# Optimization experiments

Hardware: AMD Instinct MI355X
Metric: run time of the kernel (lower is better)

Reference implementation:

```python
import jax, jax.numpy as jnp
import numpy as np
import math

B, L, D, H, FF = 8, 4096, 1024, 16, 4
BELOW, ABOVE = 1, 1
DH = D // H


def _timing_signal(length, channels, min_ts=1.0, max_ts=10000.0):
    position = np.arange(length)
    num_timescales = channels // 2
    log_inc = math.log(max_ts / min_ts) / (num_timescales - 1)
    inv = min_ts * np.exp(np.arange(num_timescales).astype(float) * -log_inc)
    scaled = position[:, None] * inv[None, :]
    sig = np.zeros((length, channels))
    sig[:, 0::2] = np.sin(scaled)
    sig[:, 1::2] = np.cos(scaled)
    return jnp.asarray(sig[None], dtype=jnp.float32)  # [1, L, D]


def setup_inputs() -> dict:
    key = jax.random.key(0)
    ks = jax.random.split(key, 8)
    s = lambda k, sh: jax.random.normal(k, sh, jnp.float32) * 0.02
    return dict(
        X=jax.random.normal(ks[0], (B, L, D), jnp.float32),
        src_mask=jnp.zeros((B, L), jnp.bool_),  # True = padding
        pe=_timing_signal(L, D),
        Wq=s(ks[1], (D, D)), Wk=s(ks[2], (D, D)), Wv=s(ks[3], (D, D)),
        bq=jnp.zeros((D,), jnp.float32), bk=jnp.zeros((D,), jnp.float32), bv=jnp.zeros((D,), jnp.float32),
        Wo=s(ks[4], (D, D)), bo=jnp.zeros((D,), jnp.float32),
        g1=jnp.ones((D,), jnp.float32), beta1=jnp.zeros((D,), jnp.float32),
        W1=s(ks[5], (D, FF * D)), b1=jnp.zeros((FF * D,), jnp.float32),
        W2=s(ks[6], (FF * D, D)), b2=jnp.zeros((D,), jnp.float32),
        g2=jnp.ones((D,), jnp.float32), beta2=jnp.zeros((D,), jnp.float32),
    )


def _layernorm(x, g, b, eps=1e-5):
    m = x.mean(-1, keepdims=True)
    v = ((x - m) ** 2).mean(-1, keepdims=True)
    return (x - m) * jax.lax.rsqrt(v + eps) * g + b


def reference(X, src_mask, pe, Wq, Wk, Wv, bq, bk, bv, Wo, bo,
              g1, beta1, W1, b1, W2, b2, g2, beta2):
    # positional encoding (dropout is identity in eval)
    X = X + pe  # [B, L, D]

    # QKV projections -> [B, L, H, DH]
    q = (X @ Wq + bq).reshape(B, L, H, DH)
    k = (X @ Wk + bk).reshape(B, L, H, DH)
    v = (X @ Wv + bv).reshape(B, L, H, DH)

    # Banded (diagonal-window) attention: query i attends keys i-BELOW..i+ABOVE.
    Wwin = BELOW + ABOVE + 1
    idx = jnp.arange(L)[:, None] + jnp.arange(-BELOW, ABOVE + 1)[None, :]  # [L, Wwin]
    valid = (idx >= 0) & (idx < L)
    idxc = jnp.clip(idx, 0, L - 1)
    kw = k[:, idxc]  # [B, L, Wwin, H, DH]
    vw = v[:, idxc]

    scores = jnp.einsum('blhd,blwhd->bhlw', q, kw) / jnp.sqrt(jnp.float32(DH))
    key_ok = ~src_mask  # [B, L]
    allow = valid[None, :, :] & key_ok[:, idxc]  # [B, L, Wwin]
    scores = jnp.where(allow[:, None, :, :], scores, jnp.float32(-1e30))
    attn = jax.nn.softmax(scores, axis=-1)  # [B, H, L, Wwin]
    ctx = jnp.einsum('bhlw,blwhd->blhd', attn, vw).reshape(B, L, D)
    Xt = ctx @ Wo + bo

    # post-norm residual blocks (dropout identity in eval)
    X = _layernorm(X + Xt, g1, beta1)
    ffn = jnp.maximum(X @ W1 + b1, 0.0) @ W2 + b2
    X = _layernorm(X + ffn, g2, beta2)
    return X
```

## Files before the change

### kernel.cpp

```cpp
#include <hip/hip_runtime.h>
#include <hip/hip_bf16.h>

#define B_  8
#define L_  4096
#define D_  1024
#define H_  16
#define MTOT (B_*L_)
#define NFF  (4*D_)

typedef __bf16 bf16_t;
typedef float  f32x4 __attribute__((ext_vector_type(4)));
typedef __bf16 b16x8 __attribute__((ext_vector_type(8)));
typedef __bf16 b16x4 __attribute__((ext_vector_type(4)));

#define OFF_WQKVT ((size_t)0)
#define OFF_WOT   ((size_t)6291456)
#define OFF_W1T   ((size_t)8388608)
#define OFF_W2T   ((size_t)16777216)
#define OFF_BQKV  ((size_t)25165824)
#define OFF_XB    ((size_t)33554432)
#define OFF_B     ((size_t)100663296)

__global__ __launch_bounds__(256) void k_add_pe(const float* __restrict__ X,
                                                const float* __restrict__ pe,
                                                bf16_t* __restrict__ Xb)
{
    size_t i  = ((size_t)blockIdx.x * 256 + threadIdx.x) * 4;
    size_t ld = i & ((size_t)L_ * D_ - 1);
    float4 x = *(const float4*)(X + i);
    float4 p = *(const float4*)(pe + ld);
    b16x4 b;
    b[0] = (bf16_t)(x.x + p.x); b[1] = (bf16_t)(x.y + p.y);
    b[2] = (bf16_t)(x.z + p.z); b[3] = (bf16_t)(x.w + p.w);
    *(b16x4*)(Xb + i) = b;
}

__global__ __launch_bounds__(256) void k_prep(const float* __restrict__ Wq,
                                              const float* __restrict__ Wk,
                                              const float* __restrict__ Wv,
                                              const float* __restrict__ Wo,
                                              const float* __restrict__ W1,
                                              const float* __restrict__ W2,
                                              const float* __restrict__ bq,
                                              const float* __restrict__ bk,
                                              const float* __restrict__ bv,
                                              bf16_t* __restrict__ WqkvT,
                                              bf16_t* __restrict__ WoT,
                                              bf16_t* __restrict__ W1T,
                                              bf16_t* __restrict__ W2T,
                                              float* __restrict__ bqkv)
{
    const int id = blockIdx.x;
    if (id >= 12288) {
        const int i = (id - 12288) * 256 + threadIdx.x;
        if (i < 1024)       bqkv[i] = bq[i];
        else if (i < 2048)  bqkv[i] = bk[i - 1024];
        else if (i < 3072)  bqkv[i] = bv[i - 2048];
        return;
    }
    const float* src; bf16_t* dst; int K, N, t;
    if (id < 4096) {
        const int w = id >> 10; t = id & 1023; K = 1024; N = 1024;
        src = (w == 0) ? Wq : (w == 1) ? Wk : (w == 2) ? Wv : Wo;
        dst = (w < 3) ? (WqkvT + (size_t)w * 1024 * 1024) : WoT;
    } else if (id < 8192) {
        t = id - 4096; K = 1024; N = 4096; src = W1; dst = W1T;
    } else {
        t = id - 8192; K = 4096; N = 1024; src = W2; dst = W2T;
    }
    const int ntiles = N >> 5;
    const int n0 = (t % ntiles) << 5;
    const int k0 = (t / ntiles) << 5;

    __shared__ float tt[32][33];
    const int tx = threadIdx.x & 31;
    const int ty = threadIdx.x >> 5;
    #pragma unroll
    for (int i = ty; i < 32; i += 8)
        tt[i][tx] = src[(size_t)(k0 + i) * N + n0 + tx];
    __syncthreads();
    #pragma unroll
    for (int i = ty; i < 32; i += 8)
        dst[(size_t)(n0 + i) * K + k0 + tx] = (bf16_t)tt[tx][i];
}

#define BM 128
#define BN 128
#define BK 64

__device__ __forceinline__ void gload_lds16(const void* g, char* lds_byte) {
    __builtin_amdgcn_global_load_lds((const __attribute__((address_space(1))) void*)g,
                                     (__attribute__((address_space(3))) void*)lds_byte,
                                     16, 0, 0);
}

template<int EPI>
__global__ __launch_bounds__(256, 4) void k_gemm_bt(const bf16_t* __restrict__ A,
                                                    const bf16_t* __restrict__ Bt,
                                                    const float* __restrict__ bias,
                                                    void* __restrict__ Cv,
                                                    const int N, const int K)
{
    __shared__ __align__(16) bf16_t As[BM * BK];
    __shared__ __align__(16) bf16_t Bs[BN * BK];
    const int tid  = threadIdx.x;
    const int wave = tid >> 6;
    const int lane = tid & 63;

    const int Nt = gridDim.x, Mt = gridDim.y;
    const int lid = blockIdx.y * Nt + blockIdx.x;
    int bm, bn;
    {
        const int xcd = lid & 7;
        const int s   = lid >> 3;
        bm = xcd * (Mt >> 3) + s / Nt;
        bn = s % Nt;
    }
    const int n0 = bn * BN;
    const int m0 = bm * BM;
    const int waveM = wave >> 1;
    const int waveN = wave & 1;

    const int srow   = tid >> 3;
    const int schunk = (tid & 7) ^ (srow & 7);
    const bf16_t* ag = A  + (size_t)(m0 + srow) * K + schunk * 8;
    const bf16_t* bg = Bt + (size_t)(n0 + srow) * K + schunk * 8;
    const size_t rstep = (size_t)32 * K;
    char* ldsA = (char*)&As[0] + wave * 1024;
    char* ldsB = (char*)&Bs[0] + wave * 1024;

    const int q   = lane >> 4;
    const int x7  = lane & 7;
    const int sl0 = ((q)     ^ x7) << 3;
    const int sl1 = ((4 + q) ^ x7) << 3;
    const bf16_t* AsP = As + (waveM * 64 + (lane & 15)) * BK;
    const bf16_t* BsP = Bs + (waveN * 64 + (lane & 15)) * BK;

    f32x4 acc[4][4] = {};

    for (int kt = 0; kt < K; kt += BK) {
        __syncthreads();
        #pragma unroll
        for (int c = 0; c < 4; ++c) {
            gload_lds16(ag + c * rstep, ldsA + c * 4096);
            gload_lds16(bg + c * rstep, ldsB + c * 4096);
        }
        ag += BK; bg += BK;
        __syncthreads();
        b16x8 af[4], bfr[4];
        #pragma unroll
        for (int i = 0; i < 4; ++i) af[i]  = *(const b16x8*)(AsP + i * 16 * BK + sl0);
        #pragma unroll
        for (int i = 0; i < 4; ++i) bfr[i] = *(const b16x8*)(BsP + i * 16 * BK + sl0);
        #pragma unroll
        for (int mi = 0; mi < 4; ++mi)
            #pragma unroll
            for (int ni = 0; ni < 4; ++ni)
                acc[mi][ni] = __builtin_amdgcn_mfma_f32_16x16x32_bf16(af[mi], bfr[ni], acc[mi][ni], 0, 0, 0);
        #pragma unroll
        for (int i = 0; i < 4; ++i) af[i]  = *(const b16x8*)(AsP + i * 16 * BK + sl1);
        #pragma unroll
        for (int i = 0; i < 4; ++i) bfr[i] = *(const b16x8*)(BsP + i * 16 * BK + sl1);
        #pragma unroll
        for (int mi = 0; mi < 4; ++mi)
            #pragma unroll
            for (int ni = 0; ni < 4; ++ni)
                acc[mi][ni] = __builtin_amdgcn_mfma_f32_16x16x32_bf16(af[mi], bfr[ni], acc[mi][ni], 0, 0, 0);
    }

    const int rbase = m0 + waveM * 64 + ((lane >> 4) << 2);
    const int cbase = n0 + waveN * 64 + (lane & 15);
    #pragma unroll
    for (int mi = 0; mi < 4; ++mi) {
        #pragma unroll
        for (int ni = 0; ni < 4; ++ni) {
            const int col = cbase + ni * 16;
            const float bb = bias[col];
            #pragma unroll
            for (int r = 0; r < 4; ++r) {
                const int rowg = rbase + mi * 16 + r;
                float v = acc[mi][ni][r] + bb;
                if (EPI == 2) v = fmaxf(v, 0.0f);
                if (EPI == 0) ((float*)Cv)[(size_t)rowg * N + col] = v;
                else          ((bf16_t*)Cv)[(size_t)rowg * N + col] = (bf16_t)v;
            }
        }
    }
}

__global__ __launch_bounds__(256) void k_attn(const bf16_t* __restrict__ QKV,
                                              const unsigned char* __restrict__ mask,
                                              bf16_t* __restrict__ ctx)
{
    const int wid  = (blockIdx.x << 2) + (threadIdx.x >> 6);
    const int lane = threadIdx.x & 63;
    const int h    = wid & (H_ - 1);
    const int l    = wid >> 4;
    const int lb   = l & (L_ - 1);

    const float qv = (float)QKV[(size_t)l * 3072 + h * 64 + lane];
    float sc[3], vv[3];
    bool  ok[3];
    #pragma unroll
    for (int w = 0; w < 3; ++w) {
        const int d   = w - 1;
        const bool valid = (unsigned)(lb + d) < (unsigned)L_;
        const int dc  = valid ? d : 0;
        const size_t rb = (size_t)(l + dc) * 3072 + h * 64 + lane;
        const float kk = (float)QKV[rb + 1024];
        vv[w] = (float)QKV[rb + 2048];
        ok[w] = valid && (mask[l + dc] == 0);
        sc[w] = qv * kk;
    }
    #pragma unroll
    for (int off = 32; off; off >>= 1) {
        sc[0] += __shfl_xor(sc[0], off);
        sc[1] += __shfl_xor(sc[1], off);
        sc[2] += __shfl_xor(sc[2], off);
    }
    const float s0 = ok[0] ? sc[0] * 0.125f : -1e30f;
    const float s1 = ok[1] ? sc[1] * 0.125f : -1e30f;
    const float s2 = ok[2] ? sc[2] * 0.125f : -1e30f;
    const float mx = fmaxf(s0, fmaxf(s1, s2));
    const float e0 = __expf(s0 - mx), e1 = __expf(s1 - mx), e2 = __expf(s2 - mx);
    const float inv = 1.0f / (e0 + e1 + e2);
    const float o = (e0 * vv[0] + e1 * vv[1] + e2 * vv[2]) * inv;
    ctx[(size_t)l * 1024 + h * 64 + lane] = (bf16_t)o;
}

template<int FINAL>
__global__ __launch_bounds__(256) void k_res_ln(const bf16_t* __restrict__ Xres,
                                                const float* __restrict__ Y,
                                                const float* __restrict__ g,
                                                const float* __restrict__ beta,
                                                bf16_t* __restrict__ outB,
                                                float* __restrict__ outF)
{
    const int row = blockIdx.x;
    const int tid = threadIdx.x;
    const size_t base = (size_t)row * D_ + tid * 4;
    b16x4  xr = *(const b16x4*)(Xres + base);
    float4 y  = *(const float4*)(Y + base);
    const float t0 = (float)xr[0] + y.x, t1 = (float)xr[1] + y.y;
    const float t2 = (float)xr[2] + y.z, t3 = (float)xr[3] + y.w;
    float s = t0 + t1 + t2 + t3;
    float q = t0*t0 + t1*t1 + t2*t2 + t3*t3;
    #pragma unroll
    for (int off = 32; off; off >>= 1) {
        s += __shfl_xor(s, off);
        q += __shfl_xor(q, off);
    }
    __shared__ float red[8];
    const int wv = tid >> 6, ln = tid & 63;
    if (ln == 0) { red[wv] = s; red[wv + 4] = q; }
    __syncthreads();
    s = red[0] + red[1] + red[2] + red[3];
    q = red[4] + red[5] + red[6] + red[7];
    const float mean = s * (1.0f / D_);
    const float var  = q * (1.0f / D_) - mean * mean;
    const float rs   = rsqrtf(var + 1e-5f);
    const int c = tid * 4;
    float4 gv = *(const float4*)(g + c);
    float4 bv = *(const float4*)(beta + c);
    float o0 = (t0 - mean) * rs * gv.x + bv.x;
    float o1 = (t1 - mean) * rs * gv.y + bv.y;
    float o2 = (t2 - mean) * rs * gv.z + bv.z;
    float o3 = (t3 - mean) * rs * gv.w + bv.w;
    if (FINAL) {
        float4 o; o.x = o0; o.y = o1; o.z = o2; o.w = o3;
        *(float4*)(outF + base) = o;
    } else {
        b16x4 b; b[0] = (bf16_t)o0; b[1] = (bf16_t)o1; b[2] = (bf16_t)o2; b[3] = (bf16_t)o3;
        *(b16x4*)(outB + base) = b;
    }
}

extern "C" void kernel_launch(void* const* d_in, const int* in_sizes, int n_in,
                              void* d_out, int out_size, void* d_ws, size_t ws_size,
                              hipStream_t stream)
{
    const float* X    = (const float*)d_in[0];
    const unsigned char* mask = (const unsigned char*)d_in[1];
    const float* pe   = (const float*)d_in[2];
    const float* Wq   = (const float*)d_in[3];
    const float* Wk   = (const float*)d_in[4];
    const float* Wv   = (const float*)d_in[5];
    const float* bq   = (const float*)d_in[6];
    const float* bk   = (const float*)d_in[7];
    const float* bv   = (const float*)d_in[8];
    const float* Wo   = (const float*)d_in[9];
    const float* bo   = (const float*)d_in[10];
    const float* g1   = (const float*)d_in[11];
    const float* be1  = (const float*)d_in[12];
    const float* W1   = (const float*)d_in[13];
    const float* b1   = (const float*)d_in[14];
    const float* W2   = (const float*)d_in[15];
    const float* b2   = (const float*)d_in[16];
    const float* g2   = (const float*)d_in[17];
    const float* be2  = (const float*)d_in[18];

    char* ws = (char*)d_ws;
    bf16_t* WqkvT = (bf16_t*)(ws + OFF_WQKVT);
    bf16_t* WoT   = (bf16_t*)(ws + OFF_WOT);
    bf16_t* W1T   = (bf16_t*)(ws + OFF_W1T);
    bf16_t* W2T   = (bf16_t*)(ws + OFF_W2T);
    float*  bqkv  = (float*) (ws + OFF_BQKV);
    bf16_t* Xb    = (bf16_t*)(ws + OFF_XB);
    float*  Y     = (float*)d_out;

    const bool big = ws_size >= (size_t)234881024;

    k_add_pe<<<MTOT * D_ / 1024, 256, 0, stream>>>(X, pe, Xb);

    k_prep<<<12300, 256, 0, stream>>>(Wq, Wk, Wv, Wo, W1, W2, bq, bk, bv,
                                      WqkvT, WoT, W1T, W2T, bqkv);

    if (big) {
        bf16_t* ctx  = (bf16_t*)(ws + OFF_B);
        bf16_t* qkvc = (bf16_t*)(ws + OFF_B + 67108864);
        for (int c = 0; c < 4; ++c) {
            const size_t r0 = (size_t)c * 8192;
            k_gemm_bt<1><<<dim3(3072/BN, 8192/BM), 256, 0, stream>>>(
                Xb + r0*D_, WqkvT, bqkv, qkvc, 3072, 1024);
            k_attn<<<8192*H_/4, 256, 0, stream>>>(qkvc, mask + r0, ctx + r0*D_);
        }
        k_gemm_bt<0><<<dim3(1024/BN, MTOT/BM), 256, 0, stream>>>(ctx, WoT, bo, Y, 1024, 1024);
        k_res_ln<0><<<MTOT, 256, 0, stream>>>(Xb, Y, g1, be1, Xb, nullptr);
        bf16_t* hb = (bf16_t*)(ws + OFF_B);
        for (int c = 0; c < 2; ++c) {
            const size_t r0 = (size_t)c * 16384;
            k_gemm_bt<2><<<dim3(NFF/BN, 16384/BM), 256, 0, stream>>>(
                Xb + r0*D_, W1T, b1, hb, NFF, 1024);
            k_gemm_bt<0><<<dim3(1024/BN, 16384/BM), 256, 0, stream>>>(
                hb, W2T, b2, Y + r0*D_, 1024, NFF);
        }
        k_res_ln<1><<<MTOT, 256, 0, stream>>>(Xb, Y, g2, be2, nullptr, (float*)d_out);
    } else {
        bf16_t* qkvc = (bf16_t*)(ws + OFF_B);
        bf16_t* ctxc = (bf16_t*)(ws + OFF_B + 25165824);
        for (int b = 0; b < B_; ++b) {
            const size_t r0 = (size_t)b * L_;
            k_gemm_bt<1><<<dim3(3072/BN, L_/BM), 256, 0, stream>>>(
                Xb + r0*D_, WqkvT, bqkv, qkvc, 3072, 1024);
            k_attn<<<L_*H_/4, 256, 0, stream>>>(qkvc, mask + r0, ctxc);
            k_gemm_bt<0><<<dim3(1024/BN, L_/BM), 256, 0, stream>>>(
                ctxc, WoT, bo, Y + r0*D_, 1024, 1024);
        }
        k_res_ln<0><<<MTOT, 256, 0, stream>>>(Xb, Y, g1, be1, Xb, nullptr);
        bf16_t* hb = (bf16_t*)(ws + OFF_B);
        for (int c = 0; c < 8; ++c) {
            const size_t r0 = (size_t)c * L_;
            k_gemm_bt<2><<<dim3(NFF/BN, L_/BM), 256, 0, stream>>>(
                Xb + r0*D_, W1T, b1, hb, NFF, 1024);
            k_gemm_bt<0><<<dim3(1024/BN, L_/BM), 256, 0, stream>>>(
                hb, W2T, b2, Y + r0*D_, 1024, NFF);
        }
        k_res_ln<1><<<MTOT, 256, 0, stream>>>(Xb, Y, g2, be2, nullptr, (float*)d_out);
    }
}
```

Measured before the change: 1.459 ms.

## Replace GEMM with 256x256 double-buffered ping-pong kernel with priority scheduling

Replaces the 128x128 single-buffered GEMM with a 256x256 tile kernel using 8 waves and 128KB of dynamic LDS. The K loop is double-buffered and split into quarter-phases, so global-to-LDS loads overlap MFMA work, with barriers and s_setprio to order the waves. The goal is more data reuse per tile and hidden load latency, at the cost of lower occupancy and tight manual vmcnt synchronisation. It also adds a one-time attribute setup for the large shared-memory size.

Result: faster. 1.332 ms (-8.7%).

```diff
diff --git a/kernel.cpp b/kernel.cpp
--- a/kernel.cpp
+++ b/kernel.cpp
@@ -84,9 +84,6 @@
         dst[(size_t)(n0 + i) * K + k0 + tx] = (bf16_t)tt[tx][i];
 }
 
-#define BM 128
-#define BN 128
-#define BK 64
 
 __device__ __forceinline__ void gload_lds16(const void* g, char* lds_byte) {
     __builtin_amdgcn_global_load_lds((const __attribute__((address_space(1))) void*)g,
@@ -94,84 +91,105 @@
                                      16, 0, 0);
 }
 
+#define GBAR() __builtin_amdgcn_s_barrier()
+#define VM4()  asm volatile("s_waitcnt vmcnt(4)" ::: "memory")
+#define PRI(x) __builtin_amdgcn_s_setprio(x)
+
 template<int EPI>
-__global__ __launch_bounds__(256, 4) void k_gemm_bt(const bf16_t* __restrict__ A,
-                                                    const bf16_t* __restrict__ Bt,
-                                                    const float* __restrict__ bias,
-                                                    void* __restrict__ Cv,
-                                                    const int N, const int K)
-{
-    __shared__ __align__(16) bf16_t As[BM * BK];
-    __shared__ __align__(16) bf16_t Bs[BN * BK];
+__global__ __launch_bounds__(512, 2) void k_g256(const bf16_t* __restrict__ A,
+                                                 const bf16_t* __restrict__ Bt,
+                                                 const float* __restrict__ bias,
+                                                 void* __restrict__ Cv,
+                                                 const int N, const int K)
+{
+    extern __shared__ char smem[];
     const int tid  = threadIdx.x;
     const int wave = tid >> 6;
     const int lane = tid & 63;
+    const int wm   = wave >> 2;
+    const int wn   = wave & 3;
 
     const int Nt = gridDim.x, Mt = gridDim.y;
     const int lid = blockIdx.y * Nt + blockIdx.x;
-    int bm, bn;
-    {
-        const int xcd = lid & 7;
-        const int s   = lid >> 3;
-        bm = xcd * (Mt >> 3) + s / Nt;
-        bn = s % Nt;
-    }
-    const int n0 = bn * BN;
-    const int m0 = bm * BM;
-    const int waveM = wave >> 1;
-    const int waveN = wave & 1;
+    const int xcd = lid & 7;
+    const int sgl = lid >> 3;
+    const int bm  = xcd * (Mt >> 3) + sgl / Nt;
+    const int bn  = sgl % Nt;
+    const int m0 = bm * 256, n0 = bn * 256;
 
     const int srow   = tid >> 3;
     const int schunk = (tid & 7) ^ (srow & 7);
-    const bf16_t* ag = A  + (size_t)(m0 + srow) * K + schunk * 8;
-    const bf16_t* bg = Bt + (size_t)(n0 + srow) * K + schunk * 8;
-    const size_t rstep = (size_t)32 * K;
-    char* ldsA = (char*)&As[0] + wave * 1024;
-    char* ldsB = (char*)&Bs[0] + wave * 1024;
-
-    const int q   = lane >> 4;
-    const int x7  = lane & 7;
-    const int sl0 = ((q)     ^ x7) << 3;
+    const bf16_t* agA = A  + (size_t)(m0 + srow) * K + schunk * 8;
+    const bf16_t* bgB = Bt + (size_t)(n0 + srow) * K + schunk * 8;
+    const size_t rstep = (size_t)64 * K;
+    const int Km1 = K - 1;
+    char* ldsw = smem + wave * 1024;
+
+    const int q  = lane >> 4, x7 = lane & 7;
+    const int sl0 = (q ^ x7) << 3;
     const int sl1 = ((4 + q) ^ x7) << 3;
-    const bf16_t* AsP = As + (waveM * 64 + (lane & 15)) * BK;
-    const bf16_t* BsP = Bs + (waveN * 64 + (lane & 15)) * BK;
-
-    f32x4 acc[4][4] = {};
-
-    for (int kt = 0; kt < K; kt += BK) {
-        __syncthreads();
-        #pragma unroll
-        for (int c = 0; c < 4; ++c) {
-            gload_lds16(ag + c * rstep, ldsA + c * 4096);
-            gload_lds16(bg + c * rstep, ldsB + c * 4096);
-        }
-        ag += BK; bg += BK;
-        __syncthreads();
-        b16x8 af[4], bfr[4];
-        #pragma unroll
-        for (int i = 0; i < 4; ++i) af[i]  = *(const b16x8*)(AsP + i * 16 * BK + sl0);
-        #pragma unroll
-        for (int i = 0; i < 4; ++i) bfr[i] = *(const b16x8*)(BsP + i * 16 * BK + sl0);
-        #pragma unroll
-        for (int mi = 0; mi < 4; ++mi)
-            #pragma unroll
-            for (int ni = 0; ni < 4; ++ni)
-                acc[mi][ni] = __builtin_amdgcn_mfma_f32_16x16x32_bf16(af[mi], bfr[ni], acc[mi][ni], 0, 0, 0);
-        #pragma unroll
-        for (int i = 0; i < 4; ++i) af[i]  = *(const b16x8*)(AsP + i * 16 * BK + sl1);
-        #pragma unroll
-        for (int i = 0; i < 4; ++i) bfr[i] = *(const b16x8*)(BsP + i * 16 * BK + sl1);
-        #pragma unroll
-        for (int mi = 0; mi < 4; ++mi)
-            #pragma unroll
-            for (int ni = 0; ni < 4; ++ni)
-                acc[mi][ni] = __builtin_amdgcn_mfma_f32_16x16x32_bf16(af[mi], bfr[ni], acc[mi][ni], 0, 0, 0);
-    }
-
-    const int rbase = m0 + waveM * 64 + ((lane >> 4) << 2);
-    const int cbase = n0 + waveN * 64 + (lane & 15);
-    #pragma unroll
-    for (int mi = 0; mi < 4; ++mi) {
+    const bf16_t* A0p = (const bf16_t*)(smem)         + (wm * 128 + (lane & 15)) * 64;
+    const bf16_t* B0p = (const bf16_t*)(smem + 32768) + (wn * 64  + (lane & 15)) * 64;
+    const bf16_t* A1p = (const bf16_t*)(smem + 65536) + (wm * 128 + (lane & 15)) * 64;
+    const bf16_t* B1p = (const bf16_t*)(smem + 98304) + (wn * 64  + (lane & 15)) * 64;
+
+    f32x4 acc[8][4] = {};
+    b16x8 aF[8], bF[8];
+
+#define STG2(gb, koff, ldsoff, pair) \
+    gload_lds16(gb + (size_t)(2*(pair)+0)*rstep + (koff), ldsw + (ldsoff) + (2*(pair)+0)*8192); \
+    gload_lds16(gb + (size_t)(2*(pair)+1)*rstep + (koff), ldsw + (ldsoff) + (2*(pair)+1)*8192)
+#define RDA(P, mh) { _Pragma("unroll") for (int ml = 0; ml < 4; ++ml) { \
+    aF[2*ml+0] = *(const b16x8*)((P) + (mh)*4096 + ml*1024 + sl0); \
+    aF[2*ml+1] = *(const b16x8*)((P) + (mh)*4096 + ml*1024 + sl1); } }
+#define RDB(P, nh) { _Pragma("unroll") for (int nl = 0; nl < 2; ++nl) { \
+    bF[2*((nh)*2+nl)+0] = *(const b16x8*)((P) + ((nh)*2+nl)*1024 + sl0); \
+    bF[2*((nh)*2+nl)+1] = *(const b16x8*)((P) + ((nh)*2+nl)*1024 + sl1); } }
+#define MM(mh, nh) { _Pragma("unroll") for (int ml = 0; ml < 4; ++ml) \
+    _Pragma("unroll") for (int nl = 0; nl < 2; ++nl) { \
+        f32x4& c = acc[(mh)*4+ml][(nh)*2+nl]; \
+        c = __builtin_amdgcn_mfma_f32_16x16x32_bf16(aF[2*ml+0], bF[2*((nh)*2+nl)+0], c, 0, 0, 0); \
+        c = __builtin_amdgcn_mfma_f32_16x16x32_bf16(aF[2*ml+1], bF[2*((nh)*2+nl)+1], c, 0, 0, 0); } }
+
+    #pragma unroll
+    for (int i = 0; i < 4; ++i) gload_lds16(agA + (size_t)i * rstep,      ldsw + 0     + i * 8192);
+    #pragma unroll
+    for (int i = 0; i < 4; ++i) gload_lds16(bgB + (size_t)i * rstep,      ldsw + 32768 + i * 8192);
+    #pragma unroll
+    for (int i = 0; i < 4; ++i) gload_lds16(bgB + (size_t)i * rstep + 64, ldsw + 98304 + i * 8192);
+    VM4();
+    GBAR();
+
+    int kb = 0;
+    const int niter = K >> 7;
+    for (int it = 0; it < niter; ++it) {
+        const int k1 = (kb +  64) & Km1;
+        const int k2 = (kb + 128) & Km1;
+        const int k3 = (kb + 192) & Km1;
+        RDA(A0p, 0); RDB(B0p, 0); STG2(agA, k1, 65536, 0);
+        GBAR(); PRI(1); MM(0, 0); PRI(0); GBAR();
+        RDB(B0p, 1);              STG2(agA, k1, 65536, 1);
+        GBAR(); PRI(1); MM(0, 1); PRI(0); GBAR();
+        RDA(A0p, 1);              STG2(bgB, k2, 32768, 0);
+        GBAR(); PRI(1); MM(1, 1); PRI(0); GBAR();
+                                  STG2(bgB, k2, 32768, 1);
+        GBAR(); PRI(1); MM(1, 0); PRI(0); VM4(); GBAR();
+        RDA(A1p, 0); RDB(B1p, 0); STG2(agA, k2, 0, 0);
+        GBAR(); PRI(1); MM(0, 0); PRI(0); GBAR();
+        RDB(B1p, 1);              STG2(agA, k2, 0, 1);
+        GBAR(); PRI(1); MM(0, 1); PRI(0); GBAR();
+        RDA(A1p, 1);              STG2(bgB, k3, 98304, 0);
+        GBAR(); PRI(1); MM(1, 1); PRI(0); GBAR();
+                                  STG2(bgB, k3, 98304, 1);
+        GBAR(); PRI(1); MM(1, 0); PRI(0); VM4(); GBAR();
+        kb = (kb + 128) & Km1;
+    }
+    asm volatile("s_waitcnt vmcnt(0)" ::: "memory");
+
+    const int rbase = m0 + wm * 128 + ((lane >> 4) << 2);
+    const int cbase = n0 + wn * 64 + (lane & 15);
+    #pragma unroll
+    for (int mi = 0; mi < 8; ++mi) {
         #pragma unroll
         for (int ni = 0; ni < 4; ++ni) {
             const int col = cbase + ni * 16;
@@ -186,6 +204,10 @@
             }
         }
     }
+#undef STG2
+#undef RDA
+#undef RDB
+#undef MM
 }
 
 __global__ __launch_bounds__(256) void k_attn(const bf16_t* __restrict__ QKV,
@@ -244,20 +266,20 @@
     const float t0 = (float)xr[0] + y.x, t1 = (float)xr[1] + y.y;
     const float t2 = (float)xr[2] + y.z, t3 = (float)xr[3] + y.w;
     float s = t0 + t1 + t2 + t3;
-    float q = t0*t0 + t1*t1 + t2*t2 + t3*t3;
+    float qq = t0*t0 + t1*t1 + t2*t2 + t3*t3;
     #pragma unroll
     for (int off = 32; off; off >>= 1) {
-        s += __shfl_xor(s, off);
-        q += __shfl_xor(q, off);
+        s  += __shfl_xor(s, off);
+        qq += __shfl_xor(qq, off);
     }
     __shared__ float red[8];
     const int wv = tid >> 6, ln = tid & 63;
-    if (ln == 0) { red[wv] = s; red[wv + 4] = q; }
+    if (ln == 0) { red[wv] = s; red[wv + 4] = qq; }
     __syncthreads();
-    s = red[0] + red[1] + red[2] + red[3];
-    q = red[4] + red[5] + red[6] + red[7];
+    s  = red[0] + red[1] + red[2] + red[3];
+    qq = red[4] + red[5] + red[6] + red[7];
     const float mean = s * (1.0f / D_);
-    const float var  = q * (1.0f / D_) - mean * mean;
+    const float var  = qq * (1.0f / D_) - mean * mean;
     const float rs   = rsqrtf(var + 1e-5f);
     const int c = tid * 4;
     float4 gv = *(const float4*)(g + c);
@@ -299,6 +321,17 @@
     const float* g2   = (const float*)d_in[17];
     const float* be2  = (const float*)d_in[18];
 
+    static int s_attr = [](){
+        (void)hipFuncSetAttribute(reinterpret_cast<const void*>(&k_g256<0>),
+                                  hipFuncAttributeMaxDynamicSharedMemorySize, 131072);
+        (void)hipFuncSetAttribute(reinterpret_cast<const void*>(&k_g256<1>),
+                                  hipFuncAttributeMaxDynamicSharedMemorySize, 131072);
+        (void)hipFuncSetAttribute(reinterpret_cast<const void*>(&k_g256<2>),
+                                  hipFuncAttributeMaxDynamicSharedMemorySize, 131072);
+        return 0;
+    }();
+    (void)s_attr;
+
     char* ws = (char*)d_ws;
     bf16_t* WqkvT = (bf16_t*)(ws + OFF_WQKVT);
     bf16_t* WoT   = (bf16_t*)(ws + OFF_WOT);
@@ -320,18 +353,18 @@
         bf16_t* qkvc = (bf16_t*)(ws + OFF_B + 67108864);
         for (int c = 0; c < 4; ++c) {
             const size_t r0 = (size_t)c * 8192;
-            k_gemm_bt<1><<<dim3(3072/BN, 8192/BM), 256, 0, stream>>>(
+            k_g256<1><<<dim3(3072/256, 8192/256), 512, 131072, stream>>>(
                 Xb + r0*D_, WqkvT, bqkv, qkvc, 3072, 1024);
             k_attn<<<8192*H_/4, 256, 0, stream>>>(qkvc, mask + r0, ctx + r0*D_);
         }
-        k_gemm_bt<0><<<dim3(1024/BN, MTOT/BM), 256, 0, stream>>>(ctx, WoT, bo, Y, 1024, 1024);
+        k_g256<0><<<dim3(1024/256, MTOT/256), 512, 131072, stream>>>(ctx, WoT, bo, Y, 1024, 1024);
         k_res_ln<0><<<MTOT, 256, 0, stream>>>(Xb, Y, g1, be1, Xb, nullptr);
         bf16_t* hb = (bf16_t*)(ws + OFF_B);
         for (int c = 0; c < 2; ++c) {
             const size_t r0 = (size_t)c * 16384;
-            k_gemm_bt<2><<<dim3(NFF/BN, 16384/BM), 256, 0, stream>>>(
+            k_g256<2><<<dim3(NFF/256, 16384/256), 512, 131072, stream>>>(
                 Xb + r0*D_, W1T, b1, hb, NFF, 1024);
-            k_gemm_bt<0><<<dim3(1024/BN, 16384/BM), 256, 0, stream>>>(
+            k_g256<0><<<dim3(1024/256, 16384/256), 512, 131072, stream>>>(
                 hb, W2T, b2, Y + r0*D_, 1024, NFF);
         }
         k_res_ln<1><<<MTOT, 256, 0, stream>>>(Xb, Y, g2, be2, nullptr, (float*)d_out);
@@ -340,19 +373,19 @@
         bf16_t* ctxc = (bf16_t*)(ws + OFF_B + 25165824);
         for (int b = 0; b < B_; ++b) {
             const size_t r0 = (size_t)b * L_;
-            k_gemm_bt<1><<<dim3(3072/BN, L_/BM), 256, 0, stream>>>(
+            k_g256<1><<<dim3(3072/256, L_/256), 512, 131072, stream>>>(
                 Xb + r0*D_, WqkvT, bqkv, qkvc, 3072, 1024);
             k_attn<<<L_*H_/4, 256, 0, stream>>>(qkvc, mask + r0, ctxc);
-            k_gemm_bt<0><<<dim3(1024/BN, L_/BM), 256, 0, stream>>>(
+            k_g256<0><<<dim3(1024/256, L_/256), 512, 131072, stream>>>(
                 ctxc, WoT, bo, Y + r0*D_, 1024, 1024);
         }
         k_res_ln<0><<<MTOT, 256, 0, stream>>>(Xb, Y, g1, be1, Xb, nullptr);
         bf16_t* hb = (bf16_t*)(ws + OFF_B);
         for (int c = 0; c < 8; ++c) {
             const size_t r0 = (size_t)c * L_;
-            k_gemm_bt<2><<<dim3(NFF/BN, L_/BM), 256, 0, stream>>>(
+            k_g256<2><<<dim3(NFF/256, L_/256), 512, 131072, stream>>>(
                 Xb + r0*D_, W1T, b1, hb, NFF, 1024);
-            k_gemm_bt<0><<<dim3(1024/BN, L_/BM), 256, 0, stream>>>(
+            k_g256<0><<<dim3(1024/256, L_/256), 512, 131072, stream>>>(
                 hb, W2T, b2, Y + r0*D_, 1024, NFF);
         }
         k_res_ln<1><<<MTOT, 256, 0, stream>>>(Xb, Y, g2, be2, nullptr, (float*)d_out);
```
